# Optimization experiments

Hardware: AMD Instinct MI355X
Metric: run time of the kernel (lower is better)

The kernel has to match this reference:

```python
import math
import jax, jax.numpy as jnp
import numpy as np

H = 16            # number_of_heads
LAYER_POS = 12    # layer_position
LAM_INIT = 0.8 - 0.6 * math.exp(-0.3 * (LAYER_POS - 1))
LN_EPS = 1e-5


def setup_inputs() -> dict:
    key = jax.random.key(0)
    ks = jax.random.split(key, 12)
    B, S, E = 2, 2048, 1024
    d = E // H
    w = 0.02  # init scale for stability
    return {
        "x":   jax.random.normal(ks[0], (B, S, E), jnp.float32),
        "Wq1": jax.random.normal(ks[1], (E, E), jnp.float32) * w,
        "Wq2": jax.random.normal(ks[2], (E, E), jnp.float32) * w,
        "Wk1": jax.random.normal(ks[3], (E, E), jnp.float32) * w,
        "Wk2": jax.random.normal(ks[4], (E, E), jnp.float32) * w,
        "Wv":  jax.random.normal(ks[5], (E, 2 * E), jnp.float32) * w,
        "Wo":  jax.random.normal(ks[6], (2 * E, E), jnp.float32) * w,
        "lq1": jax.random.normal(ks[7], (H, d), jnp.float32) * 0.1,
        "lk1": jax.random.normal(ks[8], (H, d), jnp.float32) * 0.1,
        "lq2": jax.random.normal(ks[9], (H, d), jnp.float32) * 0.1,
        "lk2": jax.random.normal(ks[10], (H, d), jnp.float32) * 0.1,
    }


def _heads(t, B, S, h, d):
    # (B,S,h*d) -> (B,h,S,d)
    return t.reshape(B, S, h, d).transpose(0, 2, 1, 3)


def reference(x, Wq1, Wq2, Wk1, Wk2, Wv, Wo, lq1, lk1, lq2, lk2):
    B, S, E = x.shape
    d = E // H
    scale = 1.0 / math.sqrt(d)

    q1 = _heads(x @ Wq1, B, S, H, d)          # (B,H,S,d)
    q2 = _heads(x @ Wq2, B, S, H, d)
    k1 = _heads(x @ Wk1, B, S, H, d)
    k2 = _heads(x @ Wk2, B, S, H, d)
    v  = _heads(x @ Wv,  B, S, H, 2 * d)       # (B,H,S,2d)

    causal = jnp.tril(jnp.ones((S, S), dtype=bool))  # (S,S)
    neg_inf = jnp.float32(-jnp.inf)

    s1 = jnp.einsum('bhqd,bhkd->bhqk', q1, k1) * scale
    s2 = jnp.einsum('bhqd,bhkd->bhqk', q2, k2) * scale
    a1 = jax.nn.softmax(jnp.where(causal, s1, neg_inf), axis=-1)
    a2 = jax.nn.softmax(jnp.where(causal, s2, neg_inf), axis=-1)

    lam = (jnp.exp(jnp.sum(lq1 * lk1, axis=-1))
           - jnp.exp(jnp.sum(lq2 * lk2, axis=-1))
           + LAM_INIT)                          # (H,)
    comb = a1 - lam[None, :, None, None] * a2   # dropout is identity in eval

    out = jnp.einsum('bhqk,bhkv->bhqv', comb, v)  # (B,H,S,2d)

    # LayerNorm over last dim (2*d), no affine
    mu = jnp.mean(out, axis=-1, keepdims=True)
    var = jnp.mean(jnp.square(out - mu), axis=-1, keepdims=True)
    normed = (out - mu) * jax.lax.rsqrt(var + LN_EPS)

    scaled = normed * (1.0 - LAM_INIT)
    merged = scaled.transpose(0, 2, 1, 3).reshape(B, S, 2 * E)
    return merged @ Wo
```

## Files before the change

kernel.cpp:

```cpp
#include <hip/hip_runtime.h>
#include <hip/hip_bf16.h>

typedef __hip_bfloat16 bf16;
typedef __bf16 bf16x8 __attribute__((ext_vector_type(8)));
typedef __bf16 bf16x4 __attribute__((ext_vector_type(4)));
typedef short  s16x4  __attribute__((ext_vector_type(4)));
typedef float  f32x4  __attribute__((ext_vector_type(4)));
typedef float  f32x16 __attribute__((ext_vector_type(16)));
typedef unsigned short ushort_t;
typedef unsigned int   uint_t;

#define NH 16
#define NB 2
#define SS 2048
#define EE 1024
#define DH 64
#define DV 128
#define PJW 6144
#define Q1O 0
#define Q2O 1024
#define K1O 2048
#define K2O 3072
#define VO  4096
#define LAM0 0.7778701f
#define LN_EPS 1e-5f
#define VSTR 68
#define SCLQ 0.18033688f

__device__ __forceinline__ void gload_lds16(const bf16* g, bf16* l) {
    __builtin_amdgcn_global_load_lds(
        (const __attribute__((address_space(1))) void*)g,
        (__attribute__((address_space(3))) void*)l, 16, 0, 0);
}

__device__ __forceinline__ void stC(float* p, float v) { *p = v; }
__device__ __forceinline__ void stC(bf16* p, float v) { *p = __float2bfloat16(v); }

#if __has_builtin(__builtin_amdgcn_mfma_f32_32x32x8_bf16)
__device__ __forceinline__ f32x16 mfma_pv(uint2 a, uint2 b, f32x16 c) {
    return __builtin_amdgcn_mfma_f32_32x32x8_bf16(
        __builtin_bit_cast(bf16x4, a), __builtin_bit_cast(bf16x4, b), c, 0, 0, 0);
}
#elif __has_builtin(__builtin_amdgcn_mfma_f32_32x32x8bf16_1k)
__device__ __forceinline__ f32x16 mfma_pv(uint2 a, uint2 b, f32x16 c) {
    return __builtin_amdgcn_mfma_f32_32x32x8bf16_1k(
        __builtin_bit_cast(s16x4, a), __builtin_bit_cast(s16x4, b), c, 0, 0, 0);
}
#else
__device__ __forceinline__ f32x16 mfma_pv(uint2 a, uint2 b, f32x16 c) {
    asm volatile("s_nop 1\n\tv_mfma_f32_32x32x8_bf16 %0, %1, %2, %0\n\ts_nop 7"
                 : "+v"(c) : "v"(a), "v"(b));
    return c;
}
#endif

__global__ __launch_bounds__(256) void transp5(const float* __restrict__ W0,
                                               const float* __restrict__ W1,
                                               const float* __restrict__ W2,
                                               const float* __restrict__ W3,
                                               const float* __restrict__ W4,
                                               bf16* __restrict__ WT) {
    __shared__ float Ts[32][33];
    const int z = blockIdx.z;
    const int bx = blockIdx.x;
    if (z < 4 && bx >= 32) return;
    const float* W = (z == 0) ? W0 : (z == 1) ? W1 : (z == 2) ? W2 : (z == 3) ? W3 : W4;
    const int N = (z == 4) ? 2048 : 1024;
    const int noff = z * 1024;
    const float scl = (z < 2) ? SCLQ : 1.0f;
    int n0 = bx * 32, k0 = blockIdx.y * 32;
    int t = threadIdx.x, tx = t & 31, ty = t >> 5;
#pragma unroll
    for (int p = 0; p < 4; ++p)
        Ts[ty + 8 * p][tx] = W[(size_t)(k0 + ty + 8 * p) * N + n0 + tx];
    __syncthreads();
#pragma unroll
    for (int p = 0; p < 4; ++p)
        WT[(size_t)(noff + n0 + ty + 8 * p) * 1024 + k0 + tx] =
            __float2bfloat16(Ts[tx][ty + 8 * p] * scl);
}

__global__ __launch_bounds__(256) void transp(const float* __restrict__ W,
                                              bf16* __restrict__ WT,
                                              int K, int N, int KST, int noff,
                                              float scl) {
    __shared__ float Ts[32][33];
    int n0 = blockIdx.x * 32, k0 = blockIdx.y * 32;
    int t = threadIdx.x, tx = t & 31, ty = t >> 5;
#pragma unroll
    for (int p = 0; p < 4; ++p)
        Ts[ty + 8 * p][tx] = W[(size_t)(k0 + ty + 8 * p) * N + n0 + tx];
    __syncthreads();
#pragma unroll
    for (int p = 0; p < 4; ++p)
        WT[(size_t)(noff + n0 + ty + 8 * p) * KST + k0 + tx] =
            __float2bfloat16(Ts[tx][ty + 8 * p] * scl);
}

template<int MODE, typename CT>
__global__ __launch_bounds__(256) void mgemm(const void* __restrict__ Ap,
                                             const bf16* __restrict__ Bt,
                                             CT* __restrict__ C,
                                             int M, int N, int K) {
    __shared__ bf16 Ahi[128][32];
    __shared__ bf16 Bs[128][32];

    const int t = threadIdx.x;
    const int w = t >> 6, l = t & 63;
    const int c = l & 15, g = l >> 4;
    const int wr = w >> 1, wc = w & 1;

    const int nwg = gridDim.x, cpx = nwg >> 3;
    const int sw = (blockIdx.x & 7) * cpx + (blockIdx.x >> 3);
    const int nbx = N >> 7;
    const int bx = sw % nbx, by = sw / nbx;
    const int row0 = by * 128, col0 = bx * 128;

    f32x4 acc[4][4];
    const f32x4 fz = {0.f, 0.f, 0.f, 0.f};
#pragma unroll
    for (int m = 0; m < 4; ++m)
#pragma unroll
        for (int n = 0; n < 4; ++n) acc[m][n] = fz;

    for (int k0 = 0; k0 < K; k0 += 32) {
        __syncthreads();
#pragma unroll
        for (int i = 0; i < 2; ++i) {
            int r = i * 64 + w * 16 + (l >> 2);
            gload_lds16(&Bt[(size_t)(col0 + r) * K + k0 + (l & 3) * 8],
                        &Bs[0][0] + (size_t)(i * 4 + w) * 512 + l * 8);
        }
        if constexpr (MODE == 1) {
            const float* A = (const float*)Ap;
#pragma unroll
            for (int i = 0; i < 4; ++i) {
                int r = (t >> 3) + 32 * i;
                const float4 v = *reinterpret_cast<const float4*>(
                    &A[(size_t)(row0 + r) * K + k0 + (t & 7) * 4]);
                float f[4] = {v.x, v.y, v.z, v.w};
                ushort_t hi[4];
#pragma unroll
                for (int j = 0; j < 4; ++j) {
                    bf16 hb = __float2bfloat16(f[j]);
                    hi[j] = *reinterpret_cast<ushort_t*>(&hb);
                }
                uint2 hp;
                hp.x = (unsigned)hi[0] | ((unsigned)hi[1] << 16);
                hp.y = (unsigned)hi[2] | ((unsigned)hi[3] << 16);
                *reinterpret_cast<uint2*>(&Ahi[r][(t & 7) * 4]) = hp;
            }
        } else {
            const bf16* A = (const bf16*)Ap;
#pragma unroll
            for (int i = 0; i < 2; ++i) {
                int r = i * 64 + w * 16 + (l >> 2);
                gload_lds16(&A[(size_t)(row0 + r) * K + k0 + (l & 3) * 8],
                            &Ahi[0][0] + (size_t)(i * 4 + w) * 512 + l * 8);
            }
        }
        __syncthreads();

        bf16x8 af[4], bfr[4];
#pragma unroll
        for (int m = 0; m < 4; ++m)
            af[m] = *reinterpret_cast<const bf16x8*>(&Ahi[wr * 64 + m * 16 + c][g * 8]);
#pragma unroll
        for (int n = 0; n < 4; ++n)
            bfr[n] = *reinterpret_cast<const bf16x8*>(&Bs[wc * 64 + n * 16 + c][g * 8]);
#pragma unroll
        for (int m = 0; m < 4; ++m)
#pragma unroll
            for (int n = 0; n < 4; ++n)
                acc[m][n] = __builtin_amdgcn_mfma_f32_16x16x32_bf16(af[m], bfr[n], acc[m][n], 0, 0, 0);
    }

#pragma unroll
    for (int m = 0; m < 4; ++m)
#pragma unroll
        for (int n = 0; n < 4; ++n)
#pragma unroll
            for (int r = 0; r < 4; ++r) {
                int row = row0 + wr * 64 + m * 16 + g * 4 + r;
                int col = col0 + wc * 64 + n * 16 + c;
                stC(&C[(size_t)row * N + col], acc[m][n][r]);
            }
}

__global__ __launch_bounds__(256, 2) void attn_mfma(
        const bf16* __restrict__ cp,
        const float* __restrict__ lq1, const float* __restrict__ lk1,
        const float* __restrict__ lq2, const float* __restrict__ lk2,
        bf16* __restrict__ merged) {
    __shared__ ushort_t K1s[2][64][64];
    __shared__ ushort_t K2s[2][64][64];
    __shared__ ushort_t Vt[DV][VSTR];

    const int t = threadIdx.x;
    const int w = t >> 6, l = t & 63;
    const int lane = l & 31, h2 = l >> 5;
    const int qgrp = w >> 1, strm = w & 1;

    const int bid = blockIdx.x;
    const int qt  = 31 - (bid >> 5);
    const int bh  = bid & 31;
    const int h   = bh & (NH - 1), b = bh >> 4;
    const int q0  = qt * 64;
    const int qw0 = q0 + 32 * qgrp;
    const int qg  = qw0 + lane;
    const int ntiles = qt + 1;

    float lam;
    {
        float s1 = lq1[h * DH + l] * lk1[h * DH + l];
        float s2 = lq2[h * DH + l] * lk2[h * DH + l];
#pragma unroll
        for (int m = 32; m >= 1; m >>= 1) {
            s1 += __shfl_xor(s1, m, 64);
            s2 += __shfl_xor(s2, m, 64);
        }
        lam = __expf(s1) - __expf(s2) + LAM0;
    }

    bf16x8 qf[4];
    {
        const int QO = strm ? Q2O : Q1O;
        size_t qrow = (size_t)(b * SS + qg) * PJW + h * DH;
#pragma unroll
        for (int kk = 0; kk < 4; ++kk)
            qf[kk] = *reinterpret_cast<const bf16x8*>(&cp[qrow + QO + 16 * kk + 8 * h2]);
    }

    const size_t TSTEP = (size_t)64 * PJW;
    const int u0 = t, u1 = 256 + t;
    const int r0u = u0 >> 3, jj0 = (u0 & 7) ^ (r0u & 7);
    const int r1u = u1 >> 3, jj1 = (u1 & 7) ^ (r1u & 7);
    const bf16* k1p0 = cp + (size_t)(b * SS + r0u) * PJW + h * DH + jj0 * 8 + K1O;
    const bf16* k1p1 = cp + (size_t)(b * SS + r1u) * PJW + h * DH + jj1 * 8 + K1O;
    const bf16* k2p0 = k1p0 + (K2O - K1O);
    const bf16* k2p1 = k1p1 + (K2O - K1O);
    auto stageK = [&](int buf) {
        bf16* d1 = (bf16*)&K1s[buf][0][0];
        bf16* d2 = (bf16*)&K2s[buf][0][0];
        gload_lds16(k1p0, d1 + u0 * 8);
        gload_lds16(k1p1, d1 + u1 * 8);
        gload_lds16(k2p0, d2 + u0 * 8);
        gload_lds16(k2p1, d2 + u1 * 8);
        k1p0 += TSTEP; k1p1 += TSTEP; k2p0 += TSTEP; k2p1 += TSTEP;
    };
    uint4 va[4];
    const int vk4 = (t & 15) * 4, vc8 = (t >> 4) * 8;
    const bf16* vp0 = cp + (size_t)(b * SS + vk4 + 0) * PJW + VO + h * DV + vc8;
    const bf16* vp1 = cp + (size_t)(b * SS + vk4 + 1) * PJW + VO + h * DV + vc8;
    const bf16* vp2 = cp + (size_t)(b * SS + vk4 + 2) * PJW + VO + h * DV + vc8;
    const bf16* vp3 = cp + (size_t)(b * SS + vk4 + 3) * PJW + VO + h * DV + vc8;
    auto loadV = [&]() {
        va[0] = *reinterpret_cast<const uint4*>(vp0);
        va[1] = *reinterpret_cast<const uint4*>(vp1);
        va[2] = *reinterpret_cast<const uint4*>(vp2);
        va[3] = *reinterpret_cast<const uint4*>(vp3);
        vp0 += TSTEP; vp1 += TSTEP; vp2 += TSTEP; vp3 += TSTEP;
    };

    f32x16 acc[4];
    const f32x16 fz16 = {0.f,0.f,0.f,0.f,0.f,0.f,0.f,0.f,0.f,0.f,0.f,0.f,0.f,0.f,0.f,0.f};
#pragma unroll
    for (int i = 0; i < 4; ++i) acc[i] = fz16;
    float mm = -1e30f, lsum = 0.f;

    stageK(0);
    loadV();

    for (int kt = 0; kt < ntiles; ++kt) {
        const int cur = kt & 1;
        const int k0 = kt * 64;
        const bool diag = (kt + 1 == ntiles);

        __syncthreads();
        if (kt + 1 < ntiles) stageK(cur ^ 1);
#pragma unroll
        for (int j = 0; j < 8; ++j) {
            ushort_t e0 = reinterpret_cast<const ushort_t*>(&va[0])[j];
            ushort_t e1 = reinterpret_cast<const ushort_t*>(&va[1])[j];
            ushort_t e2 = reinterpret_cast<const ushort_t*>(&va[2])[j];
            ushort_t e3 = reinterpret_cast<const ushort_t*>(&va[3])[j];
            uint2 pk;
            pk.x = (unsigned)e0 | ((unsigned)e1 << 16);
            pk.y = (unsigned)e2 | ((unsigned)e3 << 16);
            *reinterpret_cast<uint2*>(&Vt[vc8 + j][vk4]) = pk;
        }
        if (kt + 1 < ntiles) loadV();

        asm volatile("s_waitcnt lgkmcnt(0)" ::: "memory");
        __builtin_amdgcn_sched_barrier(0);
        __builtin_amdgcn_s_barrier();
        __builtin_amdgcn_sched_barrier(0);

        const ushort_t (*Ks)[64] = strm ? K2s[cur] : K1s[cur];

        f32x16 sA = fz16, sB = fz16;
        __builtin_amdgcn_s_setprio(1);
#pragma unroll
        for (int kk = 0; kk < 4; ++kk) {
            const int un = ((2 * kk + h2) ^ (lane & 7)) * 8;
            bf16x8 a0 = *reinterpret_cast<const bf16x8*>(&Ks[lane][un]);
            bf16x8 a1 = *reinterpret_cast<const bf16x8*>(&Ks[32 + lane][un]);
            sA = __builtin_amdgcn_mfma_f32_32x32x16_bf16(a0, qf[kk], sA, 0, 0, 0);
            sB = __builtin_amdgcn_mfma_f32_32x32x16_bf16(a1, qf[kk], sB, 0, 0, 0);
        }
        __builtin_amdgcn_s_setprio(0);

        float sv[32];
#pragma unroll
        for (int i = 0; i < 16; ++i) { sv[i] = sA[i]; sv[16 + i] = sB[i]; }
        if (diag) {
#pragma unroll
            for (int sb = 0; sb < 2; ++sb)
#pragma unroll
                for (int r = 0; r < 16; ++r) {
                    int key = k0 + 32 * sb + (r & 3) + 8 * (r >> 2) + 4 * h2;
                    if (key > qg) sv[16 * sb + r] = -1e30f;
                }
        }
        float tm[16];
#pragma unroll
        for (int i = 0; i < 16; ++i) tm[i] = fmaxf(sv[i], sv[16 + i]);
#pragma unroll
        for (int st = 8; st >= 1; st >>= 1)
#pragma unroll
            for (int i = 0; i < 16; ++i) if (i < st) tm[i] = fmaxf(tm[i], tm[i + st]);
        float mt = tm[0];
        mt = fmaxf(mt, __shfl_xor(mt, 32, 64));

        float f = 1.f;
        if (!__all(mt - mm <= 8.f)) {
            float mn = fmaxf(mm, mt);
            f = exp2f(mm - mn); mm = mn;
#pragma unroll
            for (int vb = 0; vb < 4; ++vb)
#pragma unroll
                for (int i = 0; i < 16; ++i) acc[vb][i] *= f;
        }

        float rs = 0.f;
        uint2 pa[8];
#pragma unroll
        for (int kc = 0; kc < 8; ++kc) {
            const int base = 16 * (kc >> 2) + 4 * (kc & 3);
            float p0 = exp2f(sv[base + 0] - mm);
            float p1 = exp2f(sv[base + 1] - mm);
            float p2 = exp2f(sv[base + 2] - mm);
            float p3 = exp2f(sv[base + 3] - mm);
            rs += (p0 + p1) + (p2 + p3);
            bf16 b0 = __float2bfloat16(p0), b1 = __float2bfloat16(p1);
            bf16 b2 = __float2bfloat16(p2), b3 = __float2bfloat16(p3);
            pa[kc].x = (uint_t)(*reinterpret_cast<ushort_t*>(&b0))
                     | ((uint_t)(*reinterpret_cast<ushort_t*>(&b1)) << 16);
            pa[kc].y = (uint_t)(*reinterpret_cast<ushort_t*>(&b2))
                     | ((uint_t)(*reinterpret_cast<ushort_t*>(&b3)) << 16);
        }
        lsum = lsum * f + rs;

        __builtin_amdgcn_s_setprio(1);
#pragma unroll
        for (int vb = 0; vb < 4; ++vb)
#pragma unroll
            for (int kc = 0; kc < 8; ++kc) {
                uint2 vf = *reinterpret_cast<const uint2*>(&Vt[32 * vb + lane][8 * kc + 4 * h2]);
                acc[vb] = mfma_pv(vf, pa[kc], acc[vb]);
            }
        __builtin_amdgcn_s_setprio(0);
    }

    lsum += __shfl_xor(lsum, 32, 64);
    const float rl = __builtin_amdgcn_rcpf(lsum);

    float (*ex)[33] = reinterpret_cast<float(*)[33]>(
        qgrp ? (void*)&K2s[0][0][0] : (void*)&K1s[0][0][0]);

    __syncthreads();
#pragma unroll
    for (int half = 0; half < 2; ++half) {
        if (strm) {
#pragma unroll
            for (int vv = 0; vv < 2; ++vv)
#pragma unroll
                for (int i = 0; i < 16; ++i)
                    ex[l][16 * vv + i] = acc[2 * half + vv][i] * rl;
        }
        __syncthreads();
        if (!strm) {
#pragma unroll
            for (int vv = 0; vv < 2; ++vv)
#pragma unroll
                for (int i = 0; i < 16; ++i)
                    acc[2 * half + vv][i] =
                        acc[2 * half + vv][i] * rl - lam * ex[l][16 * vv + i];
        }
        __syncthreads();
    }

    if (!strm) {
        float sum = 0.f;
#pragma unroll
        for (int vb = 0; vb < 4; ++vb)
#pragma unroll
            for (int i = 0; i < 16; ++i) sum += acc[vb][i];
        sum += __shfl_xor(sum, 32, 64);
        const float mu = sum * (1.f / 128.f);
        float var = 0.f;
#pragma unroll
        for (int vb = 0; vb < 4; ++vb)
#pragma unroll
            for (int i = 0; i < 16; ++i) {
                float d = acc[vb][i] - mu;
                var += d * d;
            }
        var += __shfl_xor(var, 32, 64);
        const float scl = rsqrtf(var * (1.f / 128.f) + LN_EPS) * (1.f - LAM0);

        const size_t orow = (size_t)(b * SS + qg) * (2 * EE) + h * DV;
#pragma unroll
        for (int vb = 0; vb < 4; ++vb)
#pragma unroll
            for (int rq = 0; rq < 4; ++rq) {
                bf16 o0 = __float2bfloat16((acc[vb][4 * rq + 0] - mu) * scl);
                bf16 o1 = __float2bfloat16((acc[vb][4 * rq + 1] - mu) * scl);
                bf16 o2 = __float2bfloat16((acc[vb][4 * rq + 2] - mu) * scl);
                bf16 o3 = __float2bfloat16((acc[vb][4 * rq + 3] - mu) * scl);
                uint2 pk;
                pk.x = (uint_t)(*reinterpret_cast<ushort_t*>(&o0))
                     | ((uint_t)(*reinterpret_cast<ushort_t*>(&o1)) << 16);
                pk.y = (uint_t)(*reinterpret_cast<ushort_t*>(&o2))
                     | ((uint_t)(*reinterpret_cast<ushort_t*>(&o3)) << 16);
                *reinterpret_cast<uint2*>(&merged[orow + 32 * vb + 8 * rq + 4 * h2]) = pk;
            }
    }
}

extern "C" void kernel_launch(void* const* d_in, const int* in_sizes, int n_in,
                              void* d_out, int out_size, void* d_ws, size_t ws_size,
                              hipStream_t stream) {
    (void)in_sizes; (void)n_in; (void)out_size; (void)ws_size;
    const float* x   = (const float*)d_in[0];
    const float* Wq1 = (const float*)d_in[1];
    const float* Wq2 = (const float*)d_in[2];
    const float* Wk1 = (const float*)d_in[3];
    const float* Wk2 = (const float*)d_in[4];
    const float* Wv  = (const float*)d_in[5];
    const float* Wo  = (const float*)d_in[6];
    const float* lq1 = (const float*)d_in[7];
    const float* lk1 = (const float*)d_in[8];
    const float* lq2 = (const float*)d_in[9];
    const float* lk2 = (const float*)d_in[10];
    float* out = (float*)d_out;

    char* ws = (char*)d_ws;
    const size_t MB = 1ull << 20;
    bf16* wcT = (bf16*)(ws);
    bf16* cpj = (bf16*)(ws + 16 * MB);
    bf16* mg  = (bf16*)(ws);
    bf16* woT = (bf16*)(ws + 16 * MB);

    dim3 blk(256);
    transp5<<<dim3(64, 32, 5), blk, 0, stream>>>(Wq1, Wq2, Wk1, Wk2, Wv, wcT);
    mgemm<1, bf16><<<dim3((6144 / 128) * (4096 / 128)), blk, 0, stream>>>(
        x, wcT, cpj, 4096, 6144, 1024);
    attn_mfma<<<dim3(NB * NH * (SS / 64)), blk, 0, stream>>>(
        cpj, lq1, lk1, lq2, lk2, mg);
    transp<<<dim3(32, 64), blk, 0, stream>>>(Wo, woT, 2048, 1024, 2048, 0, 1.0f);
    mgemm<0, float><<<dim3((1024 / 128) * (4096 / 128)), blk, 0, stream>>>(
        mg, woT, out, 4096, 1024, 2048);
}
```

Measured before the change: 256.6 us.

## Halve attention key tile to 32 and skip masked tiles per wave group

The key/value tile in the differential-attention kernel drops from 64 to 32 keys, which halves the K and V shared-memory buffers. The smaller footprint lets launch bounds ask for 4 blocks per CU instead of 2. Wave groups whose queries lie entirely before a key tile now skip its compute, which cuts causal-mask waste on the diagonal. The V transpose uses byte-permute instructions, and the max reduction is restructured. In exchange, there are twice as many loop iterations and barriers per block, fewer threads share the staging loads, and register pressure under the tighter occupancy bound is a risk.

```diff
diff --git a/kernel.cpp b/kernel.cpp
--- a/kernel.cpp
+++ b/kernel.cpp
@@ -24,8 +24,10 @@
 #define VO  4096
 #define LAM0 0.7778701f
 #define LN_EPS 1e-5f
-#define VSTR 68
+#define VSTR32 36
 #define SCLQ 0.18033688f
+#define PSEL_LO 0x05040100u
+#define PSEL_HI 0x07060302u
 
 __device__ __forceinline__ void gload_lds16(const bf16* g, bf16* l) {
     __builtin_amdgcn_global_load_lds(
@@ -187,14 +189,15 @@
             }
 }
 
-__global__ __launch_bounds__(256, 2) void attn_mfma(
+__global__ __launch_bounds__(256, 4) void attn_mfma(
         const bf16* __restrict__ cp,
         const float* __restrict__ lq1, const float* __restrict__ lk1,
         const float* __restrict__ lq2, const float* __restrict__ lk2,
         bf16* __restrict__ merged) {
-    __shared__ ushort_t K1s[2][64][64];
-    __shared__ ushort_t K2s[2][64][64];
-    __shared__ ushort_t Vt[DV][VSTR];
+    __shared__ ushort_t SMEM[4096 + 4096 + 4608];
+    ushort_t (*K1s)[32][64] = reinterpret_cast<ushort_t(*)[32][64]>(&SMEM[0]);
+    ushort_t (*K2s)[32][64] = reinterpret_cast<ushort_t(*)[32][64]>(&SMEM[4096]);
+    ushort_t (*Vt)[VSTR32]  = reinterpret_cast<ushort_t(*)[VSTR32]>(&SMEM[8192]);
 
     const int t = threadIdx.x;
     const int w = t >> 6, l = t & 63;
@@ -208,7 +211,7 @@
     const int q0  = qt * 64;
     const int qw0 = q0 + 32 * qgrp;
     const int qg  = qw0 + lane;
-    const int ntiles = qt + 1;
+    const int ntiles = 2 * qt + 2;
 
     float lam;
     {
@@ -231,25 +234,17 @@
             qf[kk] = *reinterpret_cast<const bf16x8*>(&cp[qrow + QO + 16 * kk + 8 * h2]);
     }
 
-    const size_t TSTEP = (size_t)64 * PJW;
-    const int u0 = t, u1 = 256 + t;
-    const int r0u = u0 >> 3, jj0 = (u0 & 7) ^ (r0u & 7);
-    const int r1u = u1 >> 3, jj1 = (u1 & 7) ^ (r1u & 7);
-    const bf16* k1p0 = cp + (size_t)(b * SS + r0u) * PJW + h * DH + jj0 * 8 + K1O;
-    const bf16* k1p1 = cp + (size_t)(b * SS + r1u) * PJW + h * DH + jj1 * 8 + K1O;
-    const bf16* k2p0 = k1p0 + (K2O - K1O);
-    const bf16* k2p1 = k1p1 + (K2O - K1O);
+    const size_t TSTEP = (size_t)32 * PJW;
+    const int ru = t >> 3, ju = (t & 7) ^ (ru & 7);
+    const bf16* k1p = cp + (size_t)(b * SS + ru) * PJW + h * DH + ju * 8 + K1O;
+    const bf16* k2p = k1p + (K2O - K1O);
     auto stageK = [&](int buf) {
-        bf16* d1 = (bf16*)&K1s[buf][0][0];
-        bf16* d2 = (bf16*)&K2s[buf][0][0];
-        gload_lds16(k1p0, d1 + u0 * 8);
-        gload_lds16(k1p1, d1 + u1 * 8);
-        gload_lds16(k2p0, d2 + u0 * 8);
-        gload_lds16(k2p1, d2 + u1 * 8);
-        k1p0 += TSTEP; k1p1 += TSTEP; k2p0 += TSTEP; k2p1 += TSTEP;
+        gload_lds16(k1p, (bf16*)&K1s[buf][0][0] + t * 8);
+        gload_lds16(k2p, (bf16*)&K2s[buf][0][0] + t * 8);
+        k1p += TSTEP; k2p += TSTEP;
     };
     uint4 va[4];
-    const int vk4 = (t & 15) * 4, vc8 = (t >> 4) * 8;
+    const int vk4 = (t & 7) * 4, vc8 = ((t >> 3) & 15) * 8;
     const bf16* vp0 = cp + (size_t)(b * SS + vk4 + 0) * PJW + VO + h * DV + vc8;
     const bf16* vp1 = cp + (size_t)(b * SS + vk4 + 1) * PJW + VO + h * DV + vc8;
     const bf16* vp2 = cp + (size_t)(b * SS + vk4 + 2) * PJW + VO + h * DV + vc8;
@@ -269,67 +264,70 @@
     float mm = -1e30f, lsum = 0.f;
 
     stageK(0);
-    loadV();
+    if (t < 128) loadV();
 
     for (int kt = 0; kt < ntiles; ++kt) {
         const int cur = kt & 1;
-        const int k0 = kt * 64;
-        const bool diag = (kt + 1 == ntiles);
+        const int k0 = kt * 32;
+        const bool active = (k0 <= qw0);
+        const bool diag   = (k0 == qw0);
 
         __syncthreads();
         if (kt + 1 < ntiles) stageK(cur ^ 1);
-#pragma unroll
-        for (int j = 0; j < 8; ++j) {
-            ushort_t e0 = reinterpret_cast<const ushort_t*>(&va[0])[j];
-            ushort_t e1 = reinterpret_cast<const ushort_t*>(&va[1])[j];
-            ushort_t e2 = reinterpret_cast<const ushort_t*>(&va[2])[j];
-            ushort_t e3 = reinterpret_cast<const ushort_t*>(&va[3])[j];
-            uint2 pk;
-            pk.x = (unsigned)e0 | ((unsigned)e1 << 16);
-            pk.y = (unsigned)e2 | ((unsigned)e3 << 16);
-            *reinterpret_cast<uint2*>(&Vt[vc8 + j][vk4]) = pk;
-        }
-        if (kt + 1 < ntiles) loadV();
+        if (t < 128) {
+            const uint_t* w0 = reinterpret_cast<const uint_t*>(&va[0]);
+            const uint_t* w1 = reinterpret_cast<const uint_t*>(&va[1]);
+            const uint_t* w2 = reinterpret_cast<const uint_t*>(&va[2]);
+            const uint_t* w3 = reinterpret_cast<const uint_t*>(&va[3]);
+#pragma unroll
+            for (int j = 0; j < 8; ++j) {
+                const int jw = j >> 1;
+                const uint_t sel = (j & 1) ? PSEL_HI : PSEL_LO;
+                uint2 pk;
+                pk.x = __builtin_amdgcn_perm(w1[jw], w0[jw], sel);
+                pk.y = __builtin_amdgcn_perm(w3[jw], w2[jw], sel);
+                *reinterpret_cast<uint2*>(&Vt[vc8 + j][vk4]) = pk;
+            }
+            if (kt + 1 < ntiles) loadV();
+        }
 
         asm volatile("s_waitcnt lgkmcnt(0)" ::: "memory");
         __builtin_amdgcn_sched_barrier(0);
         __builtin_amdgcn_s_barrier();
         __builtin_amdgcn_sched_barrier(0);
 
+        if (!active) continue;
+
         const ushort_t (*Ks)[64] = strm ? K2s[cur] : K1s[cur];
 
-        f32x16 sA = fz16, sB = fz16;
+        f32x16 sA = fz16;
         __builtin_amdgcn_s_setprio(1);
 #pragma unroll
         for (int kk = 0; kk < 4; ++kk) {
             const int un = ((2 * kk + h2) ^ (lane & 7)) * 8;
             bf16x8 a0 = *reinterpret_cast<const bf16x8*>(&Ks[lane][un]);
-            bf16x8 a1 = *reinterpret_cast<const bf16x8*>(&Ks[32 + lane][un]);
             sA = __builtin_amdgcn_mfma_f32_32x32x16_bf16(a0, qf[kk], sA, 0, 0, 0);
-            sB = __builtin_amdgcn_mfma_f32_32x32x16_bf16(a1, qf[kk], sB, 0, 0, 0);
         }
         __builtin_amdgcn_s_setprio(0);
 
-        float sv[32];
-#pragma unroll
-        for (int i = 0; i < 16; ++i) { sv[i] = sA[i]; sv[16 + i] = sB[i]; }
+        float sv[16];
+#pragma unroll
+        for (int i = 0; i < 16; ++i) sv[i] = sA[i];
         if (diag) {
 #pragma unroll
-            for (int sb = 0; sb < 2; ++sb)
-#pragma unroll
-                for (int r = 0; r < 16; ++r) {
-                    int key = k0 + 32 * sb + (r & 3) + 8 * (r >> 2) + 4 * h2;
-                    if (key > qg) sv[16 * sb + r] = -1e30f;
-                }
-        }
-        float tm[16];
-#pragma unroll
-        for (int i = 0; i < 16; ++i) tm[i] = fmaxf(sv[i], sv[16 + i]);
-#pragma unroll
-        for (int st = 8; st >= 1; st >>= 1)
-#pragma unroll
-            for (int i = 0; i < 16; ++i) if (i < st) tm[i] = fmaxf(tm[i], tm[i + st]);
-        float mt = tm[0];
+            for (int r = 0; r < 16; ++r) {
+                int key = k0 + (r & 3) + 8 * (r >> 2) + 4 * h2;
+                if (key > qg) sv[r] = -1e30f;
+            }
+        }
+        float tA[6];
+#pragma unroll
+        for (int i = 0; i < 5; ++i)
+            tA[i] = fmaxf(fmaxf(sv[3 * i], sv[3 * i + 1]), sv[3 * i + 2]);
+        tA[5] = sv[15];
+        float u0m = fmaxf(fmaxf(tA[0], tA[1]), tA[2]);
+        float u1m = fmaxf(fmaxf(tA[3], tA[4]), tA[5]);
+        float mt = fmaxf(u0m, u1m);
         mt = fmaxf(mt, __shfl_xor(mt, 32, 64));
 
         float f = 1.f;
@@ -343,10 +341,10 @@
         }
 
         float rs = 0.f;
-        uint2 pa[8];
-#pragma unroll
-        for (int kc = 0; kc < 8; ++kc) {
-            const int base = 16 * (kc >> 2) + 4 * (kc & 3);
+        uint2 pa[4];
+#pragma unroll
+        for (int kc = 0; kc < 4; ++kc) {
+            const int base = 4 * kc;
             float p0 = exp2f(sv[base + 0] - mm);
             float p1 = exp2f(sv[base + 1] - mm);
             float p2 = exp2f(sv[base + 2] - mm);
@@ -365,7 +363,7 @@
 #pragma unroll
         for (int vb = 0; vb < 4; ++vb)
 #pragma unroll
-            for (int kc = 0; kc < 8; ++kc) {
+            for (int kc = 0; kc < 4; ++kc) {
                 uint2 vf = *reinterpret_cast<const uint2*>(&Vt[32 * vb + lane][8 * kc + 4 * h2]);
                 acc[vb] = mfma_pv(vf, pa[kc], acc[vb]);
             }
@@ -375,8 +373,8 @@
     lsum += __shfl_xor(lsum, 32, 64);
     const float rl = __builtin_amdgcn_rcpf(lsum);
 
-    float (*ex)[33] = reinterpret_cast<float(*)[33]>(
-        qgrp ? (void*)&K2s[0][0][0] : (void*)&K1s[0][0][0]);
+    float* exb = reinterpret_cast<float*>(&SMEM[0]);
+    float* ex  = exb + qgrp * (64 * 33);
 
     __syncthreads();
 #pragma unroll
@@ -386,7 +384,7 @@
             for (int vv = 0; vv < 2; ++vv)
 #pragma unroll
                 for (int i = 0; i < 16; ++i)
-                    ex[l][16 * vv + i] = acc[2 * half + vv][i] * rl;
+                    ex[l * 33 + 16 * vv + i] = acc[2 * half + vv][i] * rl;
         }
         __syncthreads();
         if (!strm) {
@@ -395,7 +393,7 @@
 #pragma unroll
                 for (int i = 0; i < 16; ++i)
                     acc[2 * half + vv][i] =
-                        acc[2 * half + vv][i] * rl - lam * ex[l][16 * vv + i];
+                        acc[2 * half + vv][i] * rl - lam * ex[l * 33 + 16 * vv + i];
         }
         __syncthreads();
     }
```

After: 334.1 us. +30.2%, slower.
